# Kernel optimization log

Hardware: AMD Instinct MI355X
Metric: run time of the kernel (lower is better)

## Reference

```python
import jax, jax.numpy as jnp
import numpy as np

OUT = 7          # roi_align output size
SR = 2           # sampling_ratio
SCALE = 1.0 / 16.0
T_OUT = 16       # F.interpolate temporal target
EPS = 1e-6


def setup_inputs() -> dict:
    key = jax.random.key(0)
    ks = jax.random.split(key, 12)
    B, Cin, Cout, T, H, W = 1, 1536, 3072, 16, 14, 14
    y = jax.random.normal(ks[0], (B, Cin, T, H, W), jnp.float32)
    x_t = jax.random.normal(ks[1], (B, Cout, T, H, W), jnp.float32)
    # ROIs in 224x224 image coords (spatial_scale = 1/16): one [1,4] box per frame
    x1 = jax.random.uniform(ks[2], (T,), minval=0.0, maxval=112.0)
    y1 = jax.random.uniform(ks[3], (T,), minval=0.0, maxval=112.0)
    x2 = jnp.minimum(x1 + jax.random.uniform(ks[4], (T,), minval=80.0, maxval=112.0), 224.0)
    y2 = jnp.minimum(y1 + jax.random.uniform(ks[5], (T,), minval=80.0, maxval=112.0), 224.0)
    rois = jnp.stack([x1, y1, x2, y2], axis=-1)[:, None, :]  # [T,1,4]
    conv_w = jax.random.normal(ks[6], (Cout, Cin), jnp.float32) * 0.02
    conv_b = jax.random.normal(ks[7], (Cout,), jnp.float32) * 0.02
    gamma = 1.0 + 0.1 * jax.random.normal(ks[8], (Cout,), jnp.float32)
    beta = 0.1 * jax.random.normal(ks[9], (Cout,), jnp.float32)
    run_mean = 0.1 * jax.random.normal(ks[10], (Cout,), jnp.float32)
    run_var = jax.random.uniform(ks[11], (Cout,), minval=0.5, maxval=1.5)
    return dict(y=y, x_t=x_t, rois=rois, conv_w=conv_w, conv_b=conv_b,
                gamma=gamma, beta=beta, run_mean=run_mean, run_var=run_var)


def _bilinear_sample(img, ys, xs):
    # img: [C,H,W]; ys: [Sy]; xs: [Sx] -> [C,Sy,Sx]; torchvision roi_align semantics
    C, H, W = img.shape
    oy = (ys < -1.0) | (ys > H)
    ox = (xs < -1.0) | (xs > W)
    yc = jnp.clip(ys, 0.0, H - 1)
    xc = jnp.clip(xs, 0.0, W - 1)
    y0 = jnp.floor(yc).astype(jnp.int32)
    x0 = jnp.floor(xc).astype(jnp.int32)
    y1i = jnp.minimum(y0 + 1, H - 1)
    x1i = jnp.minimum(x0 + 1, W - 1)
    ly = yc - y0
    lx = xc - x0
    g = lambda yi, xi: img[:, yi[:, None], xi[None, :]]  # [C,Sy,Sx]
    wy0, wy1 = (1.0 - ly)[:, None], ly[:, None]
    wx0, wx1 = (1.0 - lx)[None, :], lx[None, :]
    val = (wy0 * wx0 * g(y0, x0) + wy0 * wx1 * g(y0, x1i)
           + wy1 * wx0 * g(y1i, x0) + wy1 * wx1 * g(y1i, x1i))
    mask = (~oy)[:, None] & (~ox)[None, :]
    return jnp.where(mask[None], val, 0.0)


def _roi_align(feat, boxes):
    # feat: [N,C,H,W]; boxes: [N,4] (one box per image, aligned=False, sampling_ratio=2)
    N, C, H, W = feat.shape
    b = boxes * SCALE
    bx1, by1, bx2, by2 = b[:, 0], b[:, 1], b[:, 2], b[:, 3]
    rw = jnp.maximum(bx2 - bx1, 1.0)
    rh = jnp.maximum(by2 - by1, 1.0)
    bw, bh = rw / OUT, rh / OUT
    # sample positions per bin: (bin + (i+0.5)/SR) * bin_size
    pos = (jnp.arange(OUT, dtype=jnp.float32)[:, None]
           + (jnp.arange(SR, dtype=jnp.float32)[None, :] + 0.5) / SR).reshape(-1)  # [OUT*SR]
    ys = by1[:, None] + pos[None, :] * bh[:, None]
    xs = bx1[:, None] + pos[None, :] * bw[:, None]
    vals = jax.vmap(_bilinear_sample)(feat, ys, xs)  # [N,C,OUT*SR,OUT*SR]
    return vals.reshape(N, C, OUT, SR, OUT, SR).mean(axis=(3, 5))


def reference(y, x_t, rois, conv_w, conv_b, gamma, beta, run_mean, run_var):
    B, Cout, T, Hf, Wf = x_t.shape
    # 1x1x1 Conv3d, stride (1,2,2)
    ys = y[:, :, :, ::2, ::2]                                   # [B,Cin,T,7,7]
    yp = jnp.einsum('bcthw,oc->bothw', ys, conv_w) + conv_b[None, :, None, None, None]
    # BatchNorm3d (eval, eps=1e-6) + GELU (exact)
    inv = gamma / jnp.sqrt(run_var + EPS)
    yp = (yp - run_mean[None, :, None, None, None]) * inv[None, :, None, None, None] \
         + beta[None, :, None, None, None]
    yp = jax.nn.gelu(yp, approximate=False)
    # nearest temporal interpolation to T_OUT (identity when Tin == 16)
    Tin = yp.shape[2]
    tidx = (jnp.arange(T_OUT) * Tin) // T_OUT
    yp = yp[:, :, tidx]                                          # [B,Cout,16,7,7]
    # fusion branch: roi_align over (B*T) frames
    ff = jnp.transpose(x_t, (0, 2, 1, 3, 4)).reshape(B * T, Cout, Hf, Wf)
    boxes = rois[:, 0, :]                                        # [T,4]
    mr = _roi_align(ff, boxes)                                   # [B*T,Cout,7,7]
    mr = jnp.transpose(mr.reshape(B, T, Cout, OUT, OUT), (0, 2, 1, 3, 4))
    weighted = yp * mr                                           # [B,Cout,16,7,7]
    # per-frame 7x7 scatter-write into zeros, same window logic as the torch loop
    bs = boxes * SCALE
    sxi = jnp.floor(bs[:, 0]).astype(jnp.int32)
    syi = jnp.floor(bs[:, 1]).astype(jnp.int32)
    exi = jnp.ceil(bs[:, 2]).astype(jnp.int32)
    eyi = jnp.ceil(bs[:, 3]).astype(jnp.int32)
    ml = jnp.where(sxi + 7 < 14, sxi, exi - 7)
    mt = jnp.where(syi + 7 < 14, syi, eyi - 7)
    def place(w_t, t_off, l_off):  # w_t: [B,Cout,7,7]
        z = jnp.zeros((B, Cout, Hf, Wf), w_t.dtype)
        return jax.lax.dynamic_update_slice(z, w_t, (0, 0, t_off, l_off))
    new_face = jax.vmap(place, in_axes=(2, 0, 0), out_axes=2)(weighted, mt, ml)
    return new_face + x_t
```

## Files before the change

### kernel.cpp

```cpp
#include <hip/hip_runtime.h>

#define KD 1536
#define ND 3072
#define MD 784
#define TT 16

typedef __attribute__((ext_vector_type(8))) short short8;
typedef __attribute__((ext_vector_type(4))) float floatx4;

__device__ __forceinline__ unsigned short f2bf(float f) {
    unsigned int x = __float_as_uint(f);
    unsigned int r = (x + 0x7fffu + ((x >> 16) & 1u)) >> 16;
    return (unsigned short)r;
}

__device__ __forceinline__ void gld_lds16(const unsigned short* g, unsigned short* l) {
    __builtin_amdgcn_global_load_lds((const __attribute__((address_space(1))) void*)g,
                                     (__attribute__((address_space(3))) void*)l, 16, 0, 0);
}

__global__ __launch_bounds__(256) void prep_k(const float* __restrict__ y,
                                              const float* __restrict__ x_t,
                                              const float* __restrict__ rois,
                                              const float* __restrict__ conv_w,
                                              unsigned short* __restrict__ Ap,
                                              unsigned short* __restrict__ Bp,
                                              float* __restrict__ mr) {
    __shared__ float sm[64 * 197];
    __shared__ float wx0s[14], wx1s[14], wy0s[14], wy1s[14];
    __shared__ int x0s[14], x1s[14], y0s[14], y1s[14], vxs[14], vys[14];
    const int bid = blockIdx.x;
    const int tid = threadIdx.x;

    const int t = bid / 48;
    const int o0 = (bid % 48) * 64;

    if (tid < 14) {
        float b0 = rois[t * 4 + 0] * 0.0625f, b1 = rois[t * 4 + 1] * 0.0625f;
        float b2 = rois[t * 4 + 2] * 0.0625f, b3 = rois[t * 4 + 3] * 0.0625f;
        float rw = fmaxf(b2 - b0, 1.0f), rh = fmaxf(b3 - b1, 1.0f);
        float bw = rw * (1.0f / 7.0f), bh = rh * (1.0f / 7.0f);
        int p = tid;
        float pos = (float)(p >> 1) + 0.25f + 0.5f * (float)(p & 1);
        float xs = b0 + pos * bw;
        float ysv = b1 + pos * bh;
        vxs[p] = (xs >= -1.0f && xs <= 14.0f);
        vys[p] = (ysv >= -1.0f && ysv <= 14.0f);
        float xc = fminf(fmaxf(xs, 0.0f), 13.0f);
        float yc = fminf(fmaxf(ysv, 0.0f), 13.0f);
        int x0 = (int)floorf(xc), y0 = (int)floorf(yc);
        x0s[p] = x0; y0s[p] = y0;
        x1s[p] = min(x0 + 1, 13); y1s[p] = min(y0 + 1, 13);
        float lx = xc - (float)x0, ly = yc - (float)y0;
        wx0s[p] = 1.0f - lx; wx1s[p] = lx; wy0s[p] = 1.0f - ly; wy1s[p] = ly;
    }
    for (int f = tid; f < 64 * 196; f += 256) {
        int c = f / 196, pix = f % 196;
        sm[c * 197 + pix] = x_t[(size_t)(o0 + c) * 3136 + t * 196 + pix];
    }
    __syncthreads();
    for (int item = tid; item < 64 * 49; item += 256) {
        int c = item & 63, ij = item >> 6;
        int i = ij / 7, j = ij % 7;
        const float* base = &sm[c * 197];
        float sum = 0.0f;
#pragma unroll
        for (int s = 0; s < 2; ++s) {
            int p = 2 * i + s;
#pragma unroll
            for (int u = 0; u < 2; ++u) {
                int q = 2 * j + u;
                if (vys[p] && vxs[q]) {
                    float v00 = base[y0s[p] * 14 + x0s[q]];
                    float v01 = base[y0s[p] * 14 + x1s[q]];
                    float v10 = base[y1s[p] * 14 + x0s[q]];
                    float v11 = base[y1s[p] * 14 + x1s[q]];
                    sum += wy0s[p] * (wx0s[q] * v00 + wx1s[q] * v01) +
                           wy1s[p] * (wx0s[q] * v10 + wx1s[q] * v11);
                }
            }
        }
        mr[(size_t)(t * 49 + ij) * ND + o0 + c] = 0.25f * sum;
    }

    if (bid < 384) {
        __syncthreads();
        int t2 = bid / 24, kc = bid % 24;
        for (int f = tid; f < 64 * 196; f += 256) {
            int c = f / 196, pix = f % 196;
            sm[c * 197 + pix] = y[(size_t)(kc * 64 + c) * 3136 + t2 * 196 + pix];
        }
        __syncthreads();
        for (int item = tid; item < 64 * 49; item += 256) {
            int c = item & 63, ij = item >> 6;
            int i = ij / 7, j = ij % 7;
            Ap[(size_t)(t2 * 49 + ij) * KD + kc * 64 + c] =
                f2bf(sm[c * 197 + (2 * i) * 14 + 2 * j]);
        }
    } else {
        size_t base = (size_t)(bid - 384) * 12288;
#pragma unroll
        for (int v = 0; v < 12; ++v) {
            size_t e = base + v * 1024 + tid * 4;
            float4 w4 = *(const float4*)(conv_w + e);
            ushort4 o;
            o.x = f2bf(w4.x); o.y = f2bf(w4.y); o.z = f2bf(w4.z); o.w = f2bf(w4.w);
            *(ushort4*)(Bp + e) = o;
        }
    }
}

__global__ __launch_bounds__(256, 4) void gemm_k(const unsigned short* __restrict__ Ap,
                                                 const unsigned short* __restrict__ Bp,
                                                 const float* __restrict__ cb,
                                                 const float* __restrict__ gm,
                                                 const float* __restrict__ bt,
                                                 const float* __restrict__ rm,
                                                 const float* __restrict__ rv,
                                                 const float* __restrict__ mr,
                                                 const float* __restrict__ x_t,
                                                 const float* __restrict__ rois,
                                                 float* __restrict__ out) {
    __shared__ unsigned short smem[16384];
    unsigned short* const As0 = smem;
    unsigned short* const As1 = smem + 4096;
    unsigned short* const Bs0 = smem + 8192;
    unsigned short* const Bs1 = smem + 12288;

    const int tid = threadIdx.x;
    const int n0 = blockIdx.x * 64;
    const int t = blockIdx.y;
    const int aRow0 = t * 49;
    const int wv = tid >> 6;
    const int lane = tid & 63;
    const int wm = wv >> 1, wn = wv & 1;
    const int l15 = lane & 15, quad = lane >> 4;
    const int prow = lane >> 3, pch = lane & 7;
    const int L = pch ^ (prow & 7);

    const unsigned short* gbase;
    unsigned short *lb0, *lb1;
    if (wv < 2) {
        gbase = Ap + (size_t)(aRow0 + wv * 32 + prow) * KD + L * 8;
        lb0 = &As0[(wv * 32) * 64];
        lb1 = &As1[(wv * 32) * 64];
    } else {
        gbase = Bp + (size_t)(n0 + (wv - 2) * 32 + prow) * KD + L * 8;
        lb0 = &Bs0[((wv - 2) * 32) * 64];
        lb1 = &Bs1[((wv - 2) * 32) * 64];
    }

    floatx4 acc00 = {0.f, 0.f, 0.f, 0.f}, acc01 = {0.f, 0.f, 0.f, 0.f};
    floatx4 acc10 = {0.f, 0.f, 0.f, 0.f}, acc11 = {0.f, 0.f, 0.f, 0.f};

#pragma unroll
    for (int j = 0; j < 4; ++j)
        gld_lds16(gbase + (size_t)j * 8 * KD, lb0 + j * 512);

    int p = 0;
    for (int kt = 0; kt < KD; kt += 64, p ^= 1) {
        __syncthreads();
        if (kt + 64 < KD) {
            unsigned short* lb = p ? lb0 : lb1;
            const unsigned short* gb = gbase + kt + 64;
#pragma unroll
            for (int j = 0; j < 4; ++j)
                gld_lds16(gb + (size_t)j * 8 * KD, lb + j * 512);
        }
        const unsigned short* Ab = p ? As1 : As0;
        const unsigned short* Bb = p ? Bs1 : Bs0;
#pragma unroll
        for (int ko = 0; ko < 2; ++ko) {
            int ch = ((ko * 4 + quad) ^ (l15 & 7)) * 8;
            short8 a0 = *(const short8*)(Ab + (wm * 32 + l15) * 64 + ch);
            short8 a1 = *(const short8*)(Ab + (wm * 32 + 16 + l15) * 64 + ch);
            short8 b0 = *(const short8*)(Bb + (wn * 32 + l15) * 64 + ch);
            short8 b1 = *(const short8*)(Bb + (wn * 32 + 16 + l15) * 64 + ch);
            acc00 = __builtin_amdgcn_mfma_f32_16x16x32_bf16(a0, b0, acc00, 0, 0, 0);
            acc01 = __builtin_amdgcn_mfma_f32_16x16x32_bf16(a0, b1, acc01, 0, 0, 0);
            acc10 = __builtin_amdgcn_mfma_f32_16x16x32_bf16(a1, b0, acc10, 0, 0, 0);
            acc11 = __builtin_amdgcn_mfma_f32_16x16x32_bf16(a1, b1, acc11, 0, 0, 0);
        }
    }

    __syncthreads();
    float* Wl = (float*)smem;
#pragma unroll
    for (int ni = 0; ni < 2; ++ni) {
        int cl = wn * 32 + ni * 16 + l15;
        int n = n0 + cl;
        float scale = gm[n] / sqrtf(rv[n] + 1e-6f);
        float shift = (cb[n] - rm[n]) * scale + bt[n];
#pragma unroll
        for (int mi = 0; mi < 2; ++mi) {
            floatx4 a = (ni == 0) ? (mi == 0 ? acc00 : acc10) : (mi == 0 ? acc01 : acc11);
#pragma unroll
            for (int r = 0; r < 4; ++r) {
                int m = wm * 32 + mi * 16 + quad * 4 + r;
                if (m < 49) {
                    float v = a[r] * scale + shift;
                    float g = 0.5f * v * (1.0f + erff(v * 0.70710678118654752f));
                    Wl[m * 65 + cl] = g * mr[(size_t)(aRow0 + m) * ND + n];
                }
            }
        }
    }
    __syncthreads();

    float b0 = rois[t * 4 + 0] * 0.0625f, b1 = rois[t * 4 + 1] * 0.0625f;
    float b2 = rois[t * 4 + 2] * 0.0625f, b3 = rois[t * 4 + 3] * 0.0625f;
    int sxi = (int)floorf(b0), syi = (int)floorf(b1);
    int exi = (int)ceilf(b2), eyi = (int)ceilf(b3);
    int ml = (sxi + 7 < 14) ? sxi : exi - 7;
    int mt = (syi + 7 < 14) ? syi : eyi - 7;
    ml = min(max(ml, 0), 7);
    mt = min(max(mt, 0), 7);

    for (int i4 = tid; i4 < 64 * 49; i4 += 256) {
        int c = i4 / 49, p4 = i4 % 49;
        size_t e0 = (size_t)(n0 + c) * 3136 + t * 196 + p4 * 4;
        float4 xv = *(const float4*)(x_t + e0);
        float r4[4] = {xv.x, xv.y, xv.z, xv.w};
#pragma unroll
        for (int u = 0; u < 4; ++u) {
            int pix = p4 * 4 + u;
            int h = pix / 14, w = pix % 14;
            int i = h - mt, j = w - ml;
            if (i >= 0 && i < 7 && j >= 0 && j < 7)
                r4[u] += Wl[(i * 7 + j) * 65 + c];
        }
        *(float4*)(out + e0) = make_float4(r4[0], r4[1], r4[2], r4[3]);
    }
}

extern "C" void kernel_launch(void* const* d_in, const int* in_sizes, int n_in,
                              void* d_out, int out_size, void* d_ws, size_t ws_size,
                              hipStream_t stream) {
    const float* y = (const float*)d_in[0];
    const float* x_t = (const float*)d_in[1];
    const float* rois = (const float*)d_in[2];
    const float* conv_w = (const float*)d_in[3];
    const float* cb = (const float*)d_in[4];
    const float* gm = (const float*)d_in[5];
    const float* bt = (const float*)d_in[6];
    const float* rm = (const float*)d_in[7];
    const float* rv = (const float*)d_in[8];
    float* out = (float*)d_out;

    char* ws = (char*)d_ws;
    unsigned short* Ap = (unsigned short*)ws;
    unsigned short* Bp = (unsigned short*)(ws + 2555904);
    float* mr = (float*)(ws + 2555904 + 9437184);

    prep_k<<<768, 256, 0, stream>>>(y, x_t, rois, conv_w, Ap, Bp, mr);
    gemm_k<<<dim3(ND / 64, TT), 256, 0, stream>>>(Ap, Bp, cb, gm, bt, rm, rv, mr, x_t, rois, out);
}
```

Baseline: 170.1 us.

## Fuse roi_align into GEMM epilogue and drop mr intermediate buffer

The roi_align computation moves from the prep kernel into the GEMM epilogue, which loads the x_t tile for its frame and channels into shared memory once. That tile feeds both the bilinear sampling and the residual add, and the result is scattered into the tile before being written out. This removes the mr workspace round trip and a second read of x_t. The GEMM kernel's shared memory grows to about 50KB and its occupancy hint drops from 4 to 3 blocks, and the prep kernel now reads y with float4 loads.

```diff
diff --git a/kernel.cpp b/kernel.cpp
--- a/kernel.cpp
+++ b/kernel.cpp
@@ -20,20 +20,71 @@
 }
 
 __global__ __launch_bounds__(256) void prep_k(const float* __restrict__ y,
-                                              const float* __restrict__ x_t,
-                                              const float* __restrict__ rois,
                                               const float* __restrict__ conv_w,
                                               unsigned short* __restrict__ Ap,
-                                              unsigned short* __restrict__ Bp,
-                                              float* __restrict__ mr) {
+                                              unsigned short* __restrict__ Bp) {
+    __shared__ float sm[64 * 197];
+    const int bid = blockIdx.x;
+    const int tid = threadIdx.x;
+
+    if (bid < 384) {
+        const int t2 = bid / 24, kc = bid % 24;
+        for (int i4 = tid; i4 < 64 * 49; i4 += 256) {
+            int c = i4 / 49, p4 = i4 % 49;
+            float4 v = *(const float4*)(y + (size_t)(kc * 64 + c) * 3136 + t2 * 196 + p4 * 4);
+            float* d = &sm[c * 197 + p4 * 4];
+            d[0] = v.x; d[1] = v.y; d[2] = v.z; d[3] = v.w;
+        }
+        __syncthreads();
+        for (int item = tid; item < 64 * 49; item += 256) {
+            int c = item & 63, ij = item >> 6;
+            int i = ij / 7, j = ij % 7;
+            Ap[(size_t)(t2 * 49 + ij) * KD + kc * 64 + c] =
+                f2bf(sm[c * 197 + (2 * i) * 14 + 2 * j]);
+        }
+    } else {
+        size_t base = (size_t)(bid - 384) * 12288;
+#pragma unroll
+        for (int v = 0; v < 12; ++v) {
+            size_t e = base + v * 1024 + tid * 4;
+            float4 w4 = *(const float4*)(conv_w + e);
+            ushort4 o;
+            o.x = f2bf(w4.x); o.y = f2bf(w4.y); o.z = f2bf(w4.z); o.w = f2bf(w4.w);
+            *(ushort4*)(Bp + e) = o;
+        }
+    }
+}
+
+__global__ __launch_bounds__(256, 3) void gemm_k(const unsigned short* __restrict__ Ap,
+                                                 const unsigned short* __restrict__ Bp,
+                                                 const float* __restrict__ cb,
+                                                 const float* __restrict__ gm,
+                                                 const float* __restrict__ bt,
+                                                 const float* __restrict__ rm,
+                                                 const float* __restrict__ rv,
+                                                 const float* __restrict__ x_t,
+                                                 const float* __restrict__ rois,
+                                                 float* __restrict__ out) {
     __shared__ float sm[64 * 197];
     __shared__ float wx0s[14], wx1s[14], wy0s[14], wy1s[14];
     __shared__ int x0s[14], x1s[14], y0s[14], y1s[14], vxs[14], vys[14];
-    const int bid = blockIdx.x;
+
+    unsigned short* const smem = (unsigned short*)sm;
+    unsigned short* const As0 = smem;
+    unsigned short* const As1 = smem + 4096;
+    unsigned short* const Bs0 = smem + 8192;
+    unsigned short* const Bs1 = smem + 12288;
+
     const int tid = threadIdx.x;
-
-    const int t = bid / 48;
-    const int o0 = (bid % 48) * 64;
+    const int n0 = blockIdx.x * 64;
+    const int t = blockIdx.y;
+    const int aRow0 = t * 49;
+    const int wv = tid >> 6;
+    const int lane = tid & 63;
+    const int wm = wv >> 1, wn = wv & 1;
+    const int l15 = lane & 15, quad = lane >> 4;
+    const int prow = lane >> 3, pch = lane & 7;
+    const int L = pch ^ (prow & 7);
 
     if (tid < 14) {
         float b0 = rois[t * 4 + 0] * 0.0625f, b1 = rois[t * 4 + 1] * 0.0625f;
@@ -54,89 +105,6 @@
         float lx = xc - (float)x0, ly = yc - (float)y0;
         wx0s[p] = 1.0f - lx; wx1s[p] = lx; wy0s[p] = 1.0f - ly; wy1s[p] = ly;
     }
-    for (int f = tid; f < 64 * 196; f += 256) {
-        int c = f / 196, pix = f % 196;
-        sm[c * 197 + pix] = x_t[(size_t)(o0 + c) * 3136 + t * 196 + pix];
-    }
-    __syncthreads();
-    for (int item = tid; item < 64 * 49; item += 256) {
-        int c = item & 63, ij = item >> 6;
-        int i = ij / 7, j = ij % 7;
-        const float* base = &sm[c * 197];
-        float sum = 0.0f;
-#pragma unroll
-        for (int s = 0; s < 2; ++s) {
-            int p = 2 * i + s;
-#pragma unroll
-            for (int u = 0; u < 2; ++u) {
-                int q = 2 * j + u;
-                if (vys[p] && vxs[q]) {
-                    float v00 = base[y0s[p] * 14 + x0s[q]];
-                    float v01 = base[y0s[p] * 14 + x1s[q]];
-                    float v10 = base[y1s[p] * 14 + x0s[q]];
-                    float v11 = base[y1s[p] * 14 + x1s[q]];
-                    sum += wy0s[p] * (wx0s[q] * v00 + wx1s[q] * v01) +
-                           wy1s[p] * (wx0s[q] * v10 + wx1s[q] * v11);
-                }
-            }
-        }
-        mr[(size_t)(t * 49 + ij) * ND + o0 + c] = 0.25f * sum;
-    }
-
-    if (bid < 384) {
-        __syncthreads();
-        int t2 = bid / 24, kc = bid % 24;
-        for (int f = tid; f < 64 * 196; f += 256) {
-            int c = f / 196, pix = f % 196;
-            sm[c * 197 + pix] = y[(size_t)(kc * 64 + c) * 3136 + t2 * 196 + pix];
-        }
-        __syncthreads();
-        for (int item = tid; item < 64 * 49; item += 256) {
-            int c = item & 63, ij = item >> 6;
-            int i = ij / 7, j = ij % 7;
-            Ap[(size_t)(t2 * 49 + ij) * KD + kc * 64 + c] =
-                f2bf(sm[c * 197 + (2 * i) * 14 + 2 * j]);
-        }
-    } else {
-        size_t base = (size_t)(bid - 384) * 12288;
-#pragma unroll
-        for (int v = 0; v < 12; ++v) {
-            size_t e = base + v * 1024 + tid * 4;
-            float4 w4 = *(const float4*)(conv_w + e);
-            ushort4 o;
-            o.x = f2bf(w4.x); o.y = f2bf(w4.y); o.z = f2bf(w4.z); o.w = f2bf(w4.w);
-            *(ushort4*)(Bp + e) = o;
-        }
-    }
-}
-
-__global__ __launch_bounds__(256, 4) void gemm_k(const unsigned short* __restrict__ Ap,
-                                                 const unsigned short* __restrict__ Bp,
-                                                 const float* __restrict__ cb,
-                                                 const float* __restrict__ gm,
-                                                 const float* __restrict__ bt,
-                                                 const float* __restrict__ rm,
-                                                 const float* __restrict__ rv,
-                                                 const float* __restrict__ mr,
-                                                 const float* __restrict__ x_t,
-                                                 const float* __restrict__ rois,
-                                                 float* __restrict__ out) {
-    __shared__ unsigned short smem[16384];
-    unsigned short* const As0 = smem;
-    unsigned short* const As1 = smem + 4096;
-    unsigned short* const Bs0 = smem + 8192;
-    unsigned short* const Bs1 = smem + 12288;
-
-    const int tid = threadIdx.x;
-    const int n0 = blockIdx.x * 64;
-    const int t = blockIdx.y;
-    const int aRow0 = t * 49;
-    const int wv = tid >> 6;
-    const int lane = tid & 63;
-    const int wm = wv >> 1, wn = wv & 1;
-    const int l15 = lane & 15, quad = lane >> 4;
-    const int prow = lane >> 3, pch = lane & 7;
-    const int L = pch ^ (prow & 7);
 
     const unsigned short* gbase;
     unsigned short *lb0, *lb1;
@@ -150,8 +118,11 @@
         lb1 = &Bs1[((wv - 2) * 32) * 64];
     }
 
-    floatx4 acc00 = {0.f, 0.f, 0.f, 0.f}, acc01 = {0.f, 0.f, 0.f, 0.f};
-    floatx4 acc10 = {0.f, 0.f, 0.f, 0.f}, acc11 = {0.f, 0.f, 0.f, 0.f};
+    floatx4 acc[2][2];
+    acc[0][0] = floatx4{0.f, 0.f, 0.f, 0.f};
+    acc[0][1] = floatx4{0.f, 0.f, 0.f, 0.f};
+    acc[1][0] = floatx4{0.f, 0.f, 0.f, 0.f};
+    acc[1][1] = floatx4{0.f, 0.f, 0.f, 0.f};
 
 #pragma unroll
     for (int j = 0; j < 4; ++j)
@@ -176,31 +147,57 @@
             short8 a1 = *(const short8*)(Ab + (wm * 32 + 16 + l15) * 64 + ch);
             short8 b0 = *(const short8*)(Bb + (wn * 32 + l15) * 64 + ch);
             short8 b1 = *(const short8*)(Bb + (wn * 32 + 16 + l15) * 64 + ch);
-            acc00 = __builtin_amdgcn_mfma_f32_16x16x32_bf16(a0, b0, acc00, 0, 0, 0);
-            acc01 = __builtin_amdgcn_mfma_f32_16x16x32_bf16(a0, b1, acc01, 0, 0, 0);
-            acc10 = __builtin_amdgcn_mfma_f32_16x16x32_bf16(a1, b0, acc10, 0, 0, 0);
-            acc11 = __builtin_amdgcn_mfma_f32_16x16x32_bf16(a1, b1, acc11, 0, 0, 0);
-        }
-    }
-
-    __syncthreads();
-    float* Wl = (float*)smem;
+            acc[0][0] = __builtin_amdgcn_mfma_f32_16x16x32_bf16(a0, b0, acc[0][0], 0, 0, 0);
+            acc[0][1] = __builtin_amdgcn_mfma_f32_16x16x32_bf16(a0, b1, acc[0][1], 0, 0, 0);
+            acc[1][0] = __builtin_amdgcn_mfma_f32_16x16x32_bf16(a1, b0, acc[1][0], 0, 0, 0);
+            acc[1][1] = __builtin_amdgcn_mfma_f32_16x16x32_bf16(a1, b1, acc[1][1], 0, 0, 0);
+        }
+    }
+
+    __syncthreads();
+    for (int i4 = tid; i4 < 64 * 49; i4 += 256) {
+        int c = i4 / 49, p4 = i4 % 49;
+        float4 xv = *(const float4*)(x_t + (size_t)(n0 + c) * 3136 + t * 196 + p4 * 4);
+        float* d = &sm[c * 197 + p4 * 4];
+        d[0] = xv.x; d[1] = xv.y; d[2] = xv.z; d[3] = xv.w;
+    }
+    __syncthreads();
+
 #pragma unroll
     for (int ni = 0; ni < 2; ++ni) {
-        int cl = wn * 32 + ni * 16 + l15;
-        int n = n0 + cl;
-        float scale = gm[n] / sqrtf(rv[n] + 1e-6f);
-        float shift = (cb[n] - rm[n]) * scale + bt[n];
+        const int cl = wn * 32 + ni * 16 + l15;
+        const int n = n0 + cl;
+        const float scale = gm[n] / sqrtf(rv[n] + 1e-6f);
+        const float shift = (cb[n] - rm[n]) * scale + bt[n];
+        const float* base = &sm[cl * 197];
 #pragma unroll
         for (int mi = 0; mi < 2; ++mi) {
-            floatx4 a = (ni == 0) ? (mi == 0 ? acc00 : acc10) : (mi == 0 ? acc01 : acc11);
 #pragma unroll
             for (int r = 0; r < 4; ++r) {
-                int m = wm * 32 + mi * 16 + quad * 4 + r;
+                const int m = wm * 32 + mi * 16 + quad * 4 + r;
                 if (m < 49) {
-                    float v = a[r] * scale + shift;
-                    float g = 0.5f * v * (1.0f + erff(v * 0.70710678118654752f));
-                    Wl[m * 65 + cl] = g * mr[(size_t)(aRow0 + m) * ND + n];
+                    const int i = m / 7, j = m % 7;
+                    float sum = 0.0f;
+#pragma unroll
+                    for (int s = 0; s < 2; ++s) {
+                        int pp = 2 * i + s;
+#pragma unroll
+                        for (int u = 0; u < 2; ++u) {
+                            int q = 2 * j + u;
+                            if (vys[pp] && vxs[q]) {
+                                float v00 = base[y0s[pp] * 14 + x0s[q]];
+                                float v01 = base[y0s[pp] * 14 + x1s[q]];
+                                float v10 = base[y1s[pp] * 14 + x0s[q]];
+                                float v11 = base[y1s[pp] * 14 + x1s[q]];
+                                sum += wy0s[pp] * (wx0s[q] * v00 + wx1s[q] * v01) +
+                                       wy1s[pp] * (wx0s[q] * v10 + wx1s[q] * v11);
+                            }
+                        }
+                    }
+                    const float mrv = 0.25f * sum;
+                    const float v = acc[mi][ni][r] * scale + shift;
+                    const float g = 0.5f * v * (1.0f + erff(v * 0.70710678118654752f));
+                    acc[mi][ni][r] = g * mrv;
                 }
             }
         }
@@ -216,20 +213,28 @@
     ml = min(max(ml, 0), 7);
     mt = min(max(mt, 0), 7);
 
+#pragma unroll
+    for (int ni = 0; ni < 2; ++ni) {
+        const int cl = wn * 32 + ni * 16 + l15;
+#pragma unroll
+        for (int mi = 0; mi < 2; ++mi) {
+#pragma unroll
+            for (int r = 0; r < 4; ++r) {
+                const int m = wm * 32 + mi * 16 + quad * 4 + r;
+                if (m < 49) {
+                    const int i = m / 7, j = m % 7;
+                    sm[cl * 197 + (mt + i) * 14 + (ml + j)] += acc[mi][ni][r];
+                }
+            }
+        }
+    }
+    __syncthreads();
+
     for (int i4 = tid; i4 < 64 * 49; i4 += 256) {
         int c = i4 / 49, p4 = i4 % 49;
+        const float* d = &sm[c * 197 + p4 * 4];
         size_t e0 = (size_t)(n0 + c) * 3136 + t * 196 + p4 * 4;
-        float4 xv = *(const float4*)(x_t + e0);
-        float r4[4] = {xv.x, xv.y, xv.z, xv.w};
-#pragma unroll
-        for (int u = 0; u < 4; ++u) {
-            int pix = p4 * 4 + u;
-            int h = pix / 14, w = pix % 14;
-            int i = h - mt, j = w - ml;
-            if (i >= 0 && i < 7 && j >= 0 && j < 7)
-                r4[u] += Wl[(i * 7 + j) * 65 + c];
-        }
-        *(float4*)(out + e0) = make_float4(r4[0], r4[1], r4[2], r4[3]);
+        *(float4*)(out + e0) = make_float4(d[0], d[1], d[2], d[3]);
     }
 }
 
@@ -250,8 +255,7 @@
     char* ws = (char*)d_ws;
     unsigned short* Ap = (unsigned short*)ws;
     unsigned short* Bp = (unsigned short*)(ws + 2555904);
-    float* mr = (float*)(ws + 2555904 + 9437184);
-
-    prep_k<<<768, 256, 0, stream>>>(y, x_t, rois, conv_w, Ap, Bp, mr);
-    gemm_k<<<dim3(ND / 64, TT), 256, 0, stream>>>(Ap, Bp, cb, gm, bt, rm, rv, mr, x_t, rois, out);
-}
+
+    prep_k<<<768, 256, 0, stream>>>(y, conv_w, Ap, Bp);
+    gemm_k<<<dim3(ND / 64, TT), 256, 0, stream>>>(Ap, Bp, cb, gm, bt, rm, rv, x_t, rois, out);
+}
```

Result: faster. 165.4 us (-2.7%).
